# Optimization experiments

Hardware: AMD Instinct MI355X
Metric: run time of the kernel (lower is better)

Reference implementation:

```python
import jax, jax.numpy as jnp
import numpy as np

N, F_IN, E = 16384, 512, 524288
H1, H2 = 32, 16


def gcn_conv(x, src, dst, W, b, n):
    # PyG GCNConv: linear (no bias) -> symmetric-normalized neighbor sum
    # (self-loops already appended to src/dst) -> add bias.
    deg = jnp.zeros((n,), x.dtype).at[dst].add(jnp.ones((src.shape[0],), x.dtype))
    dinv = jax.lax.rsqrt(deg)  # deg >= 1 thanks to self-loops
    norm = dinv[src] * dinv[dst]  # [E+N]
    xw = x @ W                    # [N, out]
    msg = xw[src] * norm[:, None] # gather over edges
    out = jnp.zeros((n, W.shape[1]), x.dtype).at[dst].add(msg)  # scatter-add
    return out + b


def setup_inputs() -> dict:
    key = jax.random.key(0)
    ks = jax.random.split(key, 8)
    x = jax.random.normal(ks[0], (N, F_IN), jnp.float32)
    edge_index = jax.random.randint(ks[1], (2, E), 0, N, jnp.int64)
    def glorot(k, shp):
        lim = np.sqrt(6.0 / (shp[0] + shp[1])).astype(np.float32)
        return jax.random.uniform(k, shp, jnp.float32, -lim, lim)
    return {
        "x": x,
        "edge_index": edge_index,
        "W1": glorot(ks[2], (F_IN, H1)), "b1": jnp.zeros((H1,), jnp.float32),
        "W2": glorot(ks[3], (H1, H2)),  "b2": jnp.zeros((H2,), jnp.float32),
        "W3": glorot(ks[4], (H1, H2)),  "b3": jnp.zeros((H2,), jnp.float32),
        "num_nodes": N,
    }


def reference(x, edge_index, W1, b1, W2, b2, W3, b3, num_nodes):
    n = num_nodes
    loops = jnp.arange(n, dtype=edge_index.dtype)
    src = jnp.concatenate([edge_index[0], loops])
    dst = jnp.concatenate([edge_index[1], loops])
    h1 = gcn_conv(x, src, dst, W1, b1, n)
    mu = gcn_conv(h1, src, dst, W2, b2, n)
    logvar = gcn_conv(h1, src, dst, W3, b3, n)
    z = mu  # eval mode: reparameterize returns mu, decoder dropout is a no-op
    adj = jax.nn.sigmoid(z @ z.T)  # [N, N] inner-product decode
    return adj, mu, logvar
```

## Files before the change

kernel.cpp:

```cpp
#include <hip/hip_runtime.h>
#include <hip/hip_bf16.h>

#define N_NODES 16384
#define F_IN    512
#define N_EDGE  524288
#define H1      32
#define H2      16

typedef float f32x4 __attribute__((ext_vector_type(4)));
typedef short bf16x8 __attribute__((ext_vector_type(8)));

#define OFF_CNT     0u
#define OFF_ROWPTR  16448u
#define OFF_CURSOR  32896u
#define OFF_SRCS    49344u
#define OFF_DINV    573632u
#define OFF_XW1     590080u
#define OFF_XW23    1114368u

__device__ __forceinline__ float sigf(float x) {
    float e = __expf(-x);
    return __builtin_amdgcn_rcpf(1.0f + e);
}

__device__ __forceinline__ unsigned short bf16_rne(float f) {
    unsigned u = __float_as_uint(f);
    return (unsigned short)((u + 0x7FFFu + ((u >> 16) & 1u)) >> 16);
}

__global__ __launch_bounds__(256) void hist_k(const int* __restrict__ ei,
                                              unsigned* __restrict__ cnt) {
    int e = blockIdx.x * 256 + threadIdx.x;
    atomicAdd(&cnt[ei[N_EDGE + e]], 1u);
}

__global__ __launch_bounds__(1024) void scan_k(const unsigned* __restrict__ cnt,
                                               unsigned* __restrict__ rowptr,
                                               unsigned* __restrict__ cursor,
                                               float* __restrict__ dinv) {
    const int t = threadIdx.x;
    unsigned vals[16];
    const uint4* c4 = (const uint4*)cnt;
#pragma unroll
    for (int i = 0; i < 4; ++i) {
        uint4 v = c4[t * 4 + i];
        vals[i * 4 + 0] = v.x; vals[i * 4 + 1] = v.y;
        vals[i * 4 + 2] = v.z; vals[i * 4 + 3] = v.w;
    }
    unsigned loc[16], s = 0;
#pragma unroll
    for (int i = 0; i < 16; ++i) { loc[i] = s; s += vals[i]; }

    const int lane = t & 63, w = t >> 6;
    unsigned v = s;
#pragma unroll
    for (int off = 1; off < 64; off <<= 1) {
        unsigned u = __shfl_up(v, off);
        if (lane >= off) v += u;
    }
    __shared__ unsigned wtot[16];
    if (lane == 63) wtot[w] = v;
    __syncthreads();
    if (t == 0) {
        unsigned run = 0;
#pragma unroll
        for (int i = 0; i < 16; ++i) { unsigned x = wtot[i]; wtot[i] = run; run += x; }
        rowptr[N_NODES] = run;
    }
    __syncthreads();
    unsigned base = wtot[w] + v - s;
#pragma unroll
    for (int i = 0; i < 16; ++i) {
        unsigned rp = base + loc[i];
        rowptr[t * 16 + i] = rp;
        cursor[t * 16 + i] = rp;
        dinv[t * 16 + i] = rsqrtf((float)(vals[i] + 1u));
    }
}

__global__ __launch_bounds__(256) void fill_k(const int* __restrict__ ei,
                                              unsigned* __restrict__ cursor,
                                              int* __restrict__ srcs) {
    int e = blockIdx.x * 256 + threadIdx.x;
    int d = ei[N_EDGE + e];
    unsigned p = atomicAdd(&cursor[d], 1u);
    srcs[p] = ei[e];
}

__global__ __launch_bounds__(256) void gemm1_k(const float* __restrict__ x,
                                               const float* __restrict__ W,
                                               float* __restrict__ xw) {
    int tid = blockIdx.x * 256 + threadIdx.x;
    int row = tid >> 3, cq = tid & 7;
    const float4* x4 = (const float4*)(x + (size_t)row * F_IN);
    const float4* W4 = (const float4*)W;
    float ax = 0.f, ay = 0.f, az = 0.f, aw = 0.f;
#pragma unroll 4
    for (int k4 = 0; k4 < F_IN / 4; ++k4) {
        float4 xv = x4[k4];
        float4 w0 = W4[(size_t)(4 * k4 + 0) * 8 + cq];
        float4 w1 = W4[(size_t)(4 * k4 + 1) * 8 + cq];
        float4 w2 = W4[(size_t)(4 * k4 + 2) * 8 + cq];
        float4 w3 = W4[(size_t)(4 * k4 + 3) * 8 + cq];
        ax = fmaf(xv.x, w0.x, ax); ay = fmaf(xv.x, w0.y, ay);
        az = fmaf(xv.x, w0.z, az); aw = fmaf(xv.x, w0.w, aw);
        ax = fmaf(xv.y, w1.x, ax); ay = fmaf(xv.y, w1.y, ay);
        az = fmaf(xv.y, w1.z, az); aw = fmaf(xv.y, w1.w, aw);
        ax = fmaf(xv.z, w2.x, ax); ay = fmaf(xv.z, w2.y, ay);
        az = fmaf(xv.z, w2.z, az); aw = fmaf(xv.z, w2.w, aw);
        ax = fmaf(xv.w, w3.x, ax); ay = fmaf(xv.w, w3.y, ay);
        az = fmaf(xv.w, w3.z, az); aw = fmaf(xv.w, w3.w, aw);
    }
    float4 o; o.x = ax; o.y = ay; o.z = az; o.w = aw;
    ((float4*)xw)[(size_t)row * 8 + cq] = o;
}

__global__ __launch_bounds__(256) void conv1_k(const float* __restrict__ xw1,
                                               const float* __restrict__ dinv,
                                               const int* __restrict__ srcs,
                                               const unsigned* __restrict__ rowptr,
                                               const float* __restrict__ b1,
                                               const float* __restrict__ W2,
                                               const float* __restrict__ W3,
                                               float* __restrict__ xw23) {
    const int t = threadIdx.x;
    const int node = blockIdx.x * 8 + (t >> 5);
    const int c = t & 31;
    unsigned e0 = rowptr[node], e1 = rowptr[node + 1];
    float sum = 0.f;
    for (unsigned e = e0; e < e1; ++e) {
        int s = srcs[e];
        sum = fmaf(xw1[(size_t)s * H1 + c], dinv[s], sum);
    }
    float di = dinv[node];
    float h = fmaf(di, sum, di * di * xw1[(size_t)node * H1 + c]) + b1[c];
    __shared__ float h1s[8][H1 + 1];
    h1s[t >> 5][c] = h;
    __syncthreads();
    const float* Wm = (c < H2) ? W2 : W3;
    int q = c & (H2 - 1);
    float acc = 0.f;
#pragma unroll
    for (int k = 0; k < H1; ++k) acc = fmaf(h1s[t >> 5][k], Wm[k * H2 + q], acc);
    xw23[(size_t)node * 32 + c] = acc;
}

__global__ __launch_bounds__(256) void conv2_k(const float* __restrict__ xw23,
                                               const float* __restrict__ dinv,
                                               const int* __restrict__ srcs,
                                               const unsigned* __restrict__ rowptr,
                                               const float* __restrict__ b2,
                                               const float* __restrict__ b3,
                                               float* __restrict__ out_mu,
                                               float* __restrict__ out_lv,
                                               unsigned short* __restrict__ zhl) {
    const int t = threadIdx.x;
    const int node = blockIdx.x * 8 + (t >> 5);
    const int c = t & 31;
    const int q = c & (H2 - 1);
    unsigned e0 = rowptr[node], e1 = rowptr[node + 1];
    float sum = 0.f;
    for (unsigned e = e0; e < e1; ++e) {
        int s = srcs[e];
        sum = fmaf(xw23[(size_t)s * 32 + c], dinv[s], sum);
    }
    float di = dinv[node];
    float v = fmaf(di, sum, di * di * xw23[(size_t)node * 32 + c]) +
              ((c < H2) ? b2[q] : b3[q]);
    if (c < H2) {
        out_mu[(size_t)node * H2 + q] = v;
        unsigned short hb = bf16_rne(v);
        float hf = __uint_as_float((unsigned)hb << 16);
        unsigned short lb = bf16_rne(v - hf);
        zhl[(size_t)node * 32 + q] = hb;
        zhl[(size_t)node * 32 + 16 + q] = lb;
    } else {
        out_lv[(size_t)node * H2 + q] = v;
    }
}

__global__ __launch_bounds__(256) void adj_k(const unsigned short* __restrict__ zhl,
                                             float* __restrict__ out) {
    __shared__ float tl[4][16 * 132];
    const int t = threadIdx.x;
    const int wave = t >> 6, lane = t & 63;
    const int lrow = lane & 15, g = lane >> 4;
    const int row0 = (blockIdx.y << 7) + wave * 32, col0 = blockIdx.x << 7;
    const short* zs = (const short*)zhl;
    float* L = &tl[wave][0];

    bf16x8 A0 = *(const bf16x8*)(zs + (size_t)(row0 + lrow) * 32 + g * 8);
    bf16x8 A1 = *(const bf16x8*)(zs + (size_t)(row0 + 16 + lrow) * 32 + g * 8);

    f32x4 acc[2][8];
#pragma unroll
    for (int m = 0; m < 2; ++m)
#pragma unroll
        for (int n = 0; n < 8; ++n) acc[m][n] = (f32x4){0.f, 0.f, 0.f, 0.f};

#pragma unroll
    for (int n = 0; n < 8; ++n) {
        const short* cb = zs + (size_t)(col0 + n * 16 + lrow) * 32;
        bf16x8 B1 = *(const bf16x8*)(cb + (g & 1) * 8);
        bf16x8 B2 = *(const bf16x8*)(cb + 16 + (g & 1) * 8);
        acc[0][n] = __builtin_amdgcn_mfma_f32_16x16x32_bf16(A0, B1, acc[0][n], 0, 0, 0);
        acc[0][n] = __builtin_amdgcn_mfma_f32_16x16x32_bf16(A0, B2, acc[0][n], 0, 0, 0);
        acc[1][n] = __builtin_amdgcn_mfma_f32_16x16x32_bf16(A1, B1, acc[1][n], 0, 0, 0);
        acc[1][n] = __builtin_amdgcn_mfma_f32_16x16x32_bf16(A1, B2, acc[1][n], 0, 0, 0);
    }

#pragma unroll
    for (int m = 0; m < 2; ++m) {
#pragma unroll
        for (int n = 0; n < 8; ++n)
#pragma unroll
            for (int r = 0; r < 4; ++r)
                L[(g * 4 + r) * 132 + n * 16 + lrow] = acc[m][n][r];
#pragma unroll
        for (int i = 0; i < 8; ++i) {
            int idx = i * 64 + lane;
            int rr = idx >> 5, cc = idx & 31;
            f32x4 v = *(f32x4*)&L[rr * 132 + cc * 4];
            f32x4 o;
            o.x = sigf(v.x); o.y = sigf(v.y); o.z = sigf(v.z); o.w = sigf(v.w);
            __builtin_nontemporal_store(
                o, (f32x4*)(out + (size_t)(row0 + m * 16 + rr) * N_NODES + col0 + cc * 4));
        }
    }
}

extern "C" void kernel_launch(void* const* d_in, const int* in_sizes, int n_in,
                              void* d_out, int out_size, void* d_ws, size_t ws_size,
                              hipStream_t stream) {
    const float* x  = (const float*)d_in[0];
    const int*   ei = (const int*)d_in[1];
    const float* W1 = (const float*)d_in[2];
    const float* b1 = (const float*)d_in[3];
    const float* W2 = (const float*)d_in[4];
    const float* b2 = (const float*)d_in[5];
    const float* W3 = (const float*)d_in[6];
    const float* b3 = (const float*)d_in[7];
    float* out = (float*)d_out;

    unsigned* ws   = (unsigned*)d_ws;
    unsigned* cnt    = ws + OFF_CNT;
    unsigned* rowptr = ws + OFF_ROWPTR;
    unsigned* cursor = ws + OFF_CURSOR;
    int*      srcs   = (int*)(ws + OFF_SRCS);
    float*    dinv   = (float*)(ws + OFF_DINV);
    float*    xw1    = (float*)(ws + OFF_XW1);
    float*    xw23   = (float*)(ws + OFF_XW23);
    unsigned short* zhl = (unsigned short*)(ws + OFF_XW1);

    float* out_mu = out + (size_t)N_NODES * N_NODES;
    float* out_lv = out_mu + (size_t)N_NODES * H2;

    (void)hipMemsetAsync(cnt, 0, N_NODES * sizeof(unsigned), stream);
    hist_k<<<N_EDGE / 256, 256, 0, stream>>>(ei, cnt);
    scan_k<<<1, 1024, 0, stream>>>(cnt, rowptr, cursor, dinv);
    fill_k<<<N_EDGE / 256, 256, 0, stream>>>(ei, cursor, srcs);
    gemm1_k<<<(N_NODES * 8) / 256, 256, 0, stream>>>(x, W1, xw1);
    conv1_k<<<N_NODES / 8, 256, 0, stream>>>(xw1, dinv, srcs, rowptr, b1, W2, W3, xw23);
    conv2_k<<<N_NODES / 8, 256, 0, stream>>>(xw23, dinv, srcs, rowptr, b2, b3,
                                             out_mu, out_lv, zhl);
    adj_k<<<dim3(N_NODES / 128, N_NODES / 128), 256, 0, stream>>>(zhl, out);
}
```

Baseline: 349.9 us.

## Compute transposed adj tile to store MFMA results directly without LDS transpose

The adj kernel swaps operand roles: the row-block z vectors are staged once in shared memory and used as B, and each wave's column slice is loaded as A. Each lane's four accumulator values then sit contiguously along a row, so they go straight from registers to global memory as 16-byte stores. This drops the per-wave LDS write/readback transpose. The trade-off is that each row segment is only 64 bytes wide per store group, which may coalesce less well than the old full 512-byte rows, and the nontemporal store hint is removed.

```diff
diff --git a/kernel.cpp b/kernel.cpp
--- a/kernel.cpp
+++ b/kernel.cpp
@@ -181,16 +181,27 @@
 
 __global__ __launch_bounds__(256) void adj_k(const unsigned short* __restrict__ zhl,
                                              float* __restrict__ out) {
-    __shared__ float tl[4][16 * 132];
+    __shared__ short zrs[128][40];
     const int t = threadIdx.x;
     const int wave = t >> 6, lane = t & 63;
     const int lrow = lane & 15, g = lane >> 4;
-    const int row0 = (blockIdx.y << 7) + wave * 32, col0 = blockIdx.x << 7;
+    const int row0 = blockIdx.y << 7, col0 = blockIdx.x << 7;
     const short* zs = (const short*)zhl;
-    float* L = &tl[wave][0];
-
-    bf16x8 A0 = *(const bf16x8*)(zs + (size_t)(row0 + lrow) * 32 + g * 8);
-    bf16x8 A1 = *(const bf16x8*)(zs + (size_t)(row0 + 16 + lrow) * 32 + g * 8);
+
+    {
+        int r = t >> 1, half = t & 1;
+        const uint4* src = (const uint4*)(zs + (size_t)(row0 + r) * 32);
+        uint4 a = src[half * 2 + 0];
+        uint4 b = src[half * 2 + 1];
+        uint4* dst = (uint4*)&zrs[r][half * 16];
+        dst[0] = a; dst[1] = b;
+    }
+
+    const int cbase = col0 + wave * 32;
+    bf16x8 A0 = *(const bf16x8*)(zs + (size_t)(cbase + lrow) * 32 + g * 8);
+    bf16x8 A1 = *(const bf16x8*)(zs + (size_t)(cbase + 16 + lrow) * 32 + g * 8);
+
+    __syncthreads();
 
     f32x4 acc[2][8];
 #pragma unroll
@@ -200,9 +211,9 @@
 
 #pragma unroll
     for (int n = 0; n < 8; ++n) {
-        const short* cb = zs + (size_t)(col0 + n * 16 + lrow) * 32;
-        bf16x8 B1 = *(const bf16x8*)(cb + (g & 1) * 8);
-        bf16x8 B2 = *(const bf16x8*)(cb + 16 + (g & 1) * 8);
+        const short* rb = &zrs[n * 16 + lrow][0];
+        bf16x8 B1 = *(const bf16x8*)(rb + (g & 1) * 8);
+        bf16x8 B2 = *(const bf16x8*)(rb + 16 + (g & 1) * 8);
         acc[0][n] = __builtin_amdgcn_mfma_f32_16x16x32_bf16(A0, B1, acc[0][n], 0, 0, 0);
         acc[0][n] = __builtin_amdgcn_mfma_f32_16x16x32_bf16(A0, B2, acc[0][n], 0, 0, 0);
         acc[1][n] = __builtin_amdgcn_mfma_f32_16x16x32_bf16(A1, B1, acc[1][n], 0, 0, 0);
@@ -210,21 +221,14 @@
     }
 
 #pragma unroll
-    for (int m = 0; m < 2; ++m) {
-#pragma unroll
-        for (int n = 0; n < 8; ++n)
-#pragma unroll
-            for (int r = 0; r < 4; ++r)
-                L[(g * 4 + r) * 132 + n * 16 + lrow] = acc[m][n][r];
-#pragma unroll
-        for (int i = 0; i < 8; ++i) {
-            int idx = i * 64 + lane;
-            int rr = idx >> 5, cc = idx & 31;
-            f32x4 v = *(f32x4*)&L[rr * 132 + cc * 4];
+    for (int n = 0; n < 8; ++n) {
+        size_t rowoff = (size_t)(row0 + n * 16 + lrow) * N_NODES;
+#pragma unroll
+        for (int m = 0; m < 2; ++m) {
             f32x4 o;
-            o.x = sigf(v.x); o.y = sigf(v.y); o.z = sigf(v.z); o.w = sigf(v.w);
-            __builtin_nontemporal_store(
-                o, (f32x4*)(out + (size_t)(row0 + m * 16 + rr) * N_NODES + col0 + cc * 4));
+            o.x = sigf(acc[m][n][0]); o.y = sigf(acc[m][n][1]);
+            o.z = sigf(acc[m][n][2]); o.w = sigf(acc[m][n][3]);
+            *(f32x4*)(out + rowoff + cbase + m * 16 + g * 4) = o;
         }
     }
 }
```

Result: slower. 357.7 us (+2.2%).
